# Kernel optimization log

Hardware: AMD Instinct MI355X
Metric: run time of the kernel (lower is better)

Reference implementation:

```python
import jax, jax.numpy as jnp
import numpy as np

N = 256
IN_FEATURES = 2048
OUT_FEATURES = 128
KERNEL_DIMS = 32


def setup_inputs() -> dict:
    key = jax.random.key(0)
    kx, kt = jax.random.split(key)
    x = jax.random.normal(kx, (N, IN_FEATURES), dtype=jnp.float32)
    T = jax.random.normal(kt, (IN_FEATURES, OUT_FEATURES, KERNEL_DIMS), dtype=jnp.float32)
    return {"x": x, "T": T}


def reference(x, T):
    # matrices: [N, out_features, kernel_dims]
    matrices = (x @ T.reshape(IN_FEATURES, OUT_FEATURES * KERNEL_DIMS)).reshape(
        -1, OUT_FEATURES, KERNEL_DIMS
    )
    # pairwise L1 distance over kernel dims: [N, N, out_features]
    norm = jnp.abs(matrices[None, :, :, :] - matrices[:, None, :, :]).sum(axis=3)
    # o_b[j, f] = sum_i exp(-norm[i, j, f]); includes self term exp(0)=1, as in original
    o_b = jnp.exp(-norm).sum(axis=0)  # [N, out_features]
    # mean=False in this configuration, so no division by batch size
    return jnp.concatenate((x, o_b), axis=1)  # [N, in_features + out_features]
```

## Files before the change

kernel.cpp:

```cpp
#include <hip/hip_runtime.h>
#include <hip/hip_bf16.h>
#include <stdint.h>

#define IN_F 2048
#define OUT_F 128
#define KD 32
#define NR 256
#define OC 2176
#define OD 4096
#define THRESH 32.0f
#define KSN 16
#define OPN (1024 * 256)

typedef __bf16 bf16x8 __attribute__((ext_vector_type(8)));
typedef __bf16 bf16x4 __attribute__((ext_vector_type(4)));
typedef float  f32x4  __attribute__((ext_vector_type(4)));
typedef uint16_t u16x8 __attribute__((ext_vector_type(8)));

__global__ __launch_bounds__(256, 2) void fused_kernel(const float* __restrict__ x,
                                                       const float* __restrict__ Tm,
                                                       float* __restrict__ out,
                                                       __bf16* __restrict__ Pp) {
    __shared__ __bf16 Bs[32][136];
    __shared__ __bf16 As[2][4][256][8];

    const int tid  = threadIdx.x;
    const int lane = tid & 63;
    const int wid  = tid >> 6;
    const int fr   = lane & 15, fg = lane >> 4;
    const int bid  = blockIdx.x;
    const int ks   = bid & 15;
    const int fo   = bid >> 4;
    const int k0   = ks * 128;

    {
        const int row = bid >> 1;
        const int off = (bid & 1) * 1024 + tid * 4;
        float4 v = *reinterpret_cast<const float4*>(&x[row * IN_F + off]);
        *reinterpret_cast<float4*>(&out[row * OC + off]) = v;
    }

    float4 xs[8];
    const int kslot = tid & 7;
    const int nrow8 = tid >> 3;
    #pragma unroll
    for (int p = 0; p < 8; ++p)
        xs[p] = *reinterpret_cast<const float4*>(&x[(p * 32 + nrow8) * IN_F + k0 + kslot * 4]);

    #pragma unroll 1
    for (int r = 0; r < 2; ++r) {
        const int idx = r * 256 + tid;
        const int fl  = idx & 3;
        const int kl  = idx >> 2;
        const float* src = Tm + (size_t)(k0 + kl) * OD + (fo * 4 + fl) * KD;

        float v[32];
        #pragma unroll
        for (int q = 0; q < 8; ++q) {
            f32x4 w = *reinterpret_cast<const f32x4*>(src + q * 4);
            v[q * 4]     = w[0];
            v[q * 4 + 1] = w[1];
            v[q * 4 + 2] = w[2];
            v[q * 4 + 3] = w[3];
        }

        float s1[16], d1[16];
        #pragma unroll
        for (int e = 0; e < 16; ++e) { s1[e] = v[2*e] + v[2*e+1]; d1[e] = v[2*e] - v[2*e+1]; }
        float s2[8], d2[8];
        #pragma unroll
        for (int e = 0; e < 8; ++e)  { s2[e] = s1[2*e] + s1[2*e+1]; d2[e] = s1[2*e] - s1[2*e+1]; }
        float s3[4], d3[4];
        #pragma unroll
        for (int e = 0; e < 4; ++e)  { s3[e] = s2[2*e] + s2[2*e+1]; d3[e] = s2[2*e] - s2[2*e+1]; }
        float s4[2], d4[2];
        #pragma unroll
        for (int e = 0; e < 2; ++e)  { s4[e] = s3[2*e] + s3[2*e+1]; d4[e] = s3[2*e] - s3[2*e+1]; }
        const float s5 = s4[0] + s4[1];
        const float d5 = s4[0] - s4[1];

        float pr[8];
        pr[0] = s5;
        { float s = 0.f;
          #pragma unroll
          for (int e = 0; e < 16; ++e) s += d1[e];
          pr[1] = s; }
        { float s = 0.f;
          #pragma unroll
          for (int e = 0; e < 8; ++e) s += d2[e];
          pr[2] = s; }
        pr[3] = (d3[0] + d3[1]) + (d3[2] + d3[3]);
        pr[4] = d4[0] + d4[1];
        pr[5] = d5;
        { float s = 0.f;
          #pragma unroll
          for (int g = 0; g < 8; ++g) s += d1[2*g] - d1[2*g+1];
          pr[6] = s; }
        pr[7] = s3[0] - s3[1] - s3[2] + s3[3];

        #pragma unroll
        for (int p = 0; p < 8; ++p)
            Bs[fl * 8 + p][kl] = (__bf16)pr[p];
    }

    #pragma unroll
    for (int p = 0; p < 8; ++p) {
        bf16x4 b = { (__bf16)xs[p].x, (__bf16)xs[p].y, (__bf16)xs[p].z, (__bf16)xs[p].w };
        *reinterpret_cast<bf16x4*>(&As[0][kslot >> 1][p * 32 + nrow8][(kslot & 1) * 4]) = b;
    }
    __syncthreads();

    f32x4 acc[4][2] = {};

    #pragma unroll 1
    for (int c = 0; c < 4; ++c) {
        const int buf = c & 1;
        if (c < 3) {
            #pragma unroll
            for (int p = 0; p < 8; ++p)
                xs[p] = *reinterpret_cast<const float4*>(
                    &x[(p * 32 + nrow8) * IN_F + k0 + (c + 1) * 32 + kslot * 4]);
        }

        bf16x8 bfrag[2];
        #pragma unroll
        for (int oi = 0; oi < 2; ++oi)
            bfrag[oi] = *reinterpret_cast<const bf16x8*>(&Bs[oi * 16 + fr][c * 32 + fg * 8]);
        #pragma unroll
        for (int mi = 0; mi < 4; ++mi) {
            bf16x8 af = *reinterpret_cast<const bf16x8*>(&As[buf][fg][wid * 64 + mi * 16 + fr][0]);
            acc[mi][0] = __builtin_amdgcn_mfma_f32_16x16x32_bf16(af, bfrag[0], acc[mi][0], 0, 0, 0);
            acc[mi][1] = __builtin_amdgcn_mfma_f32_16x16x32_bf16(af, bfrag[1], acc[mi][1], 0, 0, 0);
        }

        if (c < 3) {
            __syncthreads();
            #pragma unroll
            for (int p = 0; p < 8; ++p) {
                bf16x4 b = { (__bf16)xs[p].x, (__bf16)xs[p].y, (__bf16)xs[p].z, (__bf16)xs[p].w };
                *reinterpret_cast<bf16x4*>(&As[buf ^ 1][kslot >> 1][p * 32 + nrow8][(kslot & 1) * 4]) = b;
            }
            __syncthreads();
        }
    }

    __bf16* dst = Pp + (size_t)ks * OPN;
    #pragma unroll
    for (int mi = 0; mi < 4; ++mi) {
        #pragma unroll
        for (int oi = 0; oi < 2; ++oi) {
            const int op = fo * 32 + oi * 16 + fr;
            const int nb = wid * 64 + mi * 16 + fg * 4;
            bf16x4 v = { (__bf16)acc[mi][oi][0], (__bf16)acc[mi][oi][1],
                         (__bf16)acc[mi][oi][2], (__bf16)acc[mi][oi][3] };
            *reinterpret_cast<bf16x4*>(&dst[(size_t)op * NR + nb]) = v;
        }
    }
}

__global__ __launch_bounds__(256, 2) void screen_kernel(const __bf16* __restrict__ Pp,
                                                        const float* __restrict__ x,
                                                        const float* __restrict__ Tm,
                                                        float* __restrict__ out) {
    __shared__ float P8s[256][8];
    __shared__ float part[4][64];

    const int f    = blockIdx.x;
    const int jq   = blockIdx.y;
    const int tid  = threadIdx.x;
    const int lane = tid & 63;
    const int wid  = tid >> 6;
    const int j    = jq * 64 + lane;

    {
        const int p  = tid >> 5;
        const int n0 = (tid & 31) * 8;
        const uint16_t* base = reinterpret_cast<const uint16_t*>(Pp)
                             + (size_t)(f * 8 + p) * NR + n0;
        float a[8] = {};
        #pragma unroll
        for (int ks = 0; ks < KSN; ++ks) {
            u16x8 v = *reinterpret_cast<const u16x8*>(base + (size_t)ks * OPN);
            #pragma unroll
            for (int e = 0; e < 8; ++e)
                a[e] += __builtin_bit_cast(float, (uint32_t)v[e] << 16);
        }
        #pragma unroll
        for (int e = 0; e < 8; ++e)
            P8s[n0 + e][p] = a[e];
    }
    __syncthreads();

    const f32x4 qj0 = *reinterpret_cast<const f32x4*>(&P8s[j][0]);
    const f32x4 qj1 = *reinterpret_cast<const f32x4*>(&P8s[j][4]);

    float acc = 0.f;
    const int i0 = wid * 64;
    #pragma unroll 2
    for (int ii = 0; ii < 64; ++ii) {
        const int i = i0 + ii;
        f32x4 r0 = *reinterpret_cast<const f32x4*>(&P8s[i][0]);
        f32x4 r1 = *reinterpret_cast<const f32x4*>(&P8s[i][4]);
        f32x4 d0 = r0 - qj0;
        f32x4 d1 = r1 - qj1;
        float m0 = fmaxf(fmaxf(fabsf(d0[0]), fabsf(d0[1])), fabsf(d0[2]));
        float m1 = fmaxf(fmaxf(fabsf(d0[3]), fabsf(d1[0])), fabsf(d1[1]));
        float m2 = fmaxf(fabsf(d1[2]), fabsf(d1[3]));
        const float mx = fmaxf(fmaxf(m0, m1), m2);

        const bool ok = (mx < THRESH) && (i != j);
        if (__builtin_expect(__any(ok), 0)) {
            if (ok) {
                f32x4 ad[8] = {};
                const float* xi = x + (size_t)i * IN_F;
                const float* xj = x + (size_t)j * IN_F;
                for (int k = 0; k < IN_F; ++k) {
                    const float dk = xi[k] - xj[k];
                    const float* tr = Tm + (size_t)k * OD + f * KD;
                    #pragma unroll
                    for (int q = 0; q < 8; ++q) {
                        f32x4 tv = *reinterpret_cast<const f32x4*>(tr + q * 4);
                        ad[q] += dk * tv;
                    }
                }
                float norm = 0.f;
                #pragma unroll
                for (int q = 0; q < 8; ++q)
                    norm += fabsf(ad[q][0]) + fabsf(ad[q][1])
                          + fabsf(ad[q][2]) + fabsf(ad[q][3]);
                acc += __expf(-norm);
            }
        }
    }

    if (wid == jq) acc += 1.0f;

    part[wid][lane] = acc;
    __syncthreads();
    if (tid < 64) {
        float s = part[0][tid] + part[1][tid] + part[2][tid] + part[3][tid];
        out[(jq * 64 + tid) * OC + IN_F + f] = s;
    }
}

extern "C" void kernel_launch(void* const* d_in, const int* in_sizes, int n_in,
                              void* d_out, int out_size, void* d_ws, size_t ws_size,
                              hipStream_t stream) {
    const float* x  = (const float*)d_in[0];
    const float* Tm = (const float*)d_in[1];
    float* out = (float*)d_out;

    __bf16* Pp = (__bf16*)d_ws;

    fused_kernel<<<dim3(512), 256, 0, stream>>>(x, Tm, out, Pp);
    screen_kernel<<<dim3(128, 4), 256, 0, stream>>>(Pp, x, Tm, out);
}
```

Baseline: 28.48 us.

## Halve per-block feature tile, double grid, load x fragments directly from global

Each block of the fused kernel now covers 2 features (16 projection columns) rather than 4, and the grid doubles to 1024 blocks with launch bounds raised to 4 blocks per CU. The double-buffered LDS staging of x and its barriers are removed; each wave instead reads x straight from global memory and converts it to bf16 just before each MFMA. The Bs writes are rotated per feature to reduce LDS bank conflicts. This aims at more parallelism and fewer synchronisations, in exchange for redundant global reads of x across blocks and possibly less coalesced access.

```diff
diff --git a/kernel.cpp b/kernel.cpp
--- a/kernel.cpp
+++ b/kernel.cpp
@@ -17,12 +17,43 @@
 typedef float  f32x4  __attribute__((ext_vector_type(4)));
 typedef uint16_t u16x8 __attribute__((ext_vector_type(8)));
 
-__global__ __launch_bounds__(256, 2) void fused_kernel(const float* __restrict__ x,
+__device__ __forceinline__ void bfly8(const float v[32], float pr[8]) {
+    float s1[16], d1[16];
+    #pragma unroll
+    for (int e = 0; e < 16; ++e) { s1[e] = v[2*e] + v[2*e+1]; d1[e] = v[2*e] - v[2*e+1]; }
+    float s2[8], d2[8];
+    #pragma unroll
+    for (int e = 0; e < 8; ++e)  { s2[e] = s1[2*e] + s1[2*e+1]; d2[e] = s1[2*e] - s1[2*e+1]; }
+    float s3[4], d3[4];
+    #pragma unroll
+    for (int e = 0; e < 4; ++e)  { s3[e] = s2[2*e] + s2[2*e+1]; d3[e] = s2[2*e] - s2[2*e+1]; }
+    float s4[2], d4[2];
+    #pragma unroll
+    for (int e = 0; e < 2; ++e)  { s4[e] = s3[2*e] + s3[2*e+1]; d4[e] = s3[2*e] - s3[2*e+1]; }
+    pr[0] = s4[0] + s4[1];
+    { float s = 0.f;
+      #pragma unroll
+      for (int e = 0; e < 16; ++e) s += d1[e];
+      pr[1] = s; }
+    { float s = 0.f;
+      #pragma unroll
+      for (int e = 0; e < 8; ++e) s += d2[e];
+      pr[2] = s; }
+    pr[3] = (d3[0] + d3[1]) + (d3[2] + d3[3]);
+    pr[4] = d4[0] + d4[1];
+    pr[5] = s4[0] - s4[1];
+    { float s = 0.f;
+      #pragma unroll
+      for (int g = 0; g < 8; ++g) s += d1[2*g] - d1[2*g+1];
+      pr[6] = s; }
+    pr[7] = s3[0] - s3[1] - s3[2] + s3[3];
+}
+
+__global__ __launch_bounds__(256, 4) void fused_kernel(const float* __restrict__ x,
                                                        const float* __restrict__ Tm,
                                                        float* __restrict__ out,
                                                        __bf16* __restrict__ Pp) {
-    __shared__ __bf16 Bs[32][136];
-    __shared__ __bf16 As[2][4][256][8];
+    __shared__ __bf16 Bs[16][136];
 
     const int tid  = threadIdx.x;
     const int lane = tid & 63;
@@ -33,126 +64,61 @@
     const int fo   = bid >> 4;
     const int k0   = ks * 128;
 
-    {
+    if (bid < 512) {
         const int row = bid >> 1;
         const int off = (bid & 1) * 1024 + tid * 4;
         float4 v = *reinterpret_cast<const float4*>(&x[row * IN_F + off]);
         *reinterpret_cast<float4*>(&out[row * OC + off]) = v;
     }
 
-    float4 xs[8];
-    const int kslot = tid & 7;
-    const int nrow8 = tid >> 3;
-    #pragma unroll
-    for (int p = 0; p < 8; ++p)
-        xs[p] = *reinterpret_cast<const float4*>(&x[(p * 32 + nrow8) * IN_F + k0 + kslot * 4]);
-
-    #pragma unroll 1
-    for (int r = 0; r < 2; ++r) {
-        const int idx = r * 256 + tid;
-        const int fl  = idx & 3;
-        const int kl  = idx >> 2;
-        const float* src = Tm + (size_t)(k0 + kl) * OD + (fo * 4 + fl) * KD;
+    {
+        const int fl = tid & 1;
+        const int kl = tid >> 1;
+        const float* src = Tm + (size_t)(k0 + kl) * OD + (fo * 2 + fl) * KD;
 
         float v[32];
         #pragma unroll
         for (int q = 0; q < 8; ++q) {
             f32x4 w = *reinterpret_cast<const f32x4*>(src + q * 4);
-            v[q * 4]     = w[0];
-            v[q * 4 + 1] = w[1];
-            v[q * 4 + 2] = w[2];
-            v[q * 4 + 3] = w[3];
-        }
-
-        float s1[16], d1[16];
-        #pragma unroll
-        for (int e = 0; e < 16; ++e) { s1[e] = v[2*e] + v[2*e+1]; d1[e] = v[2*e] - v[2*e+1]; }
-        float s2[8], d2[8];
-        #pragma unroll
-        for (int e = 0; e < 8; ++e)  { s2[e] = s1[2*e] + s1[2*e+1]; d2[e] = s1[2*e] - s1[2*e+1]; }
-        float s3[4], d3[4];
-        #pragma unroll
-        for (int e = 0; e < 4; ++e)  { s3[e] = s2[2*e] + s2[2*e+1]; d3[e] = s2[2*e] - s2[2*e+1]; }
-        float s4[2], d4[2];
-        #pragma unroll
-        for (int e = 0; e < 2; ++e)  { s4[e] = s3[2*e] + s3[2*e+1]; d4[e] = s3[2*e] - s3[2*e+1]; }
-        const float s5 = s4[0] + s4[1];
-        const float d5 = s4[0] - s4[1];
+            v[q*4] = w[0]; v[q*4+1] = w[1]; v[q*4+2] = w[2]; v[q*4+3] = w[3];
+        }
 
         float pr[8];
-        pr[0] = s5;
-        { float s = 0.f;
-          #pragma unroll
-          for (int e = 0; e < 16; ++e) s += d1[e];
-          pr[1] = s; }
-        { float s = 0.f;
-          #pragma unroll
-          for (int e = 0; e < 8; ++e) s += d2[e];
-          pr[2] = s; }
-        pr[3] = (d3[0] + d3[1]) + (d3[2] + d3[3]);
-        pr[4] = d4[0] + d4[1];
-        pr[5] = d5;
-        { float s = 0.f;
-          #pragma unroll
-          for (int g = 0; g < 8; ++g) s += d1[2*g] - d1[2*g+1];
-          pr[6] = s; }
-        pr[7] = s3[0] - s3[1] - s3[2] + s3[3];
-
-        #pragma unroll
-        for (int p = 0; p < 8; ++p)
+        bfly8(v, pr);
+
+        #pragma unroll
+        for (int pp = 0; pp < 8; ++pp) {
+            const int p = (pp + fl * 4) & 7;
             Bs[fl * 8 + p][kl] = (__bf16)pr[p];
-    }
-
-    #pragma unroll
-    for (int p = 0; p < 8; ++p) {
-        bf16x4 b = { (__bf16)xs[p].x, (__bf16)xs[p].y, (__bf16)xs[p].z, (__bf16)xs[p].w };
-        *reinterpret_cast<bf16x4*>(&As[0][kslot >> 1][p * 32 + nrow8][(kslot & 1) * 4]) = b;
+        }
     }
     __syncthreads();
 
-    f32x4 acc[4][2] = {};
-
-    #pragma unroll 1
+    f32x4 acc[4] = {};
+
+    #pragma unroll
     for (int c = 0; c < 4; ++c) {
-        const int buf = c & 1;
-        if (c < 3) {
-            #pragma unroll
-            for (int p = 0; p < 8; ++p)
-                xs[p] = *reinterpret_cast<const float4*>(
-                    &x[(p * 32 + nrow8) * IN_F + k0 + (c + 1) * 32 + kslot * 4]);
-        }
-
-        bf16x8 bfrag[2];
-        #pragma unroll
-        for (int oi = 0; oi < 2; ++oi)
-            bfrag[oi] = *reinterpret_cast<const bf16x8*>(&Bs[oi * 16 + fr][c * 32 + fg * 8]);
+        const bf16x8 bfrag = *reinterpret_cast<const bf16x8*>(&Bs[fr][c * 32 + fg * 8]);
         #pragma unroll
         for (int mi = 0; mi < 4; ++mi) {
-            bf16x8 af = *reinterpret_cast<const bf16x8*>(&As[buf][fg][wid * 64 + mi * 16 + fr][0]);
-            acc[mi][0] = __builtin_amdgcn_mfma_f32_16x16x32_bf16(af, bfrag[0], acc[mi][0], 0, 0, 0);
-            acc[mi][1] = __builtin_amdgcn_mfma_f32_16x16x32_bf16(af, bfrag[1], acc[mi][1], 0, 0, 0);
-        }
-
-        if (c < 3) {
-            __syncthreads();
-            #pragma unroll
-            for (int p = 0; p < 8; ++p) {
-                bf16x4 b = { (__bf16)xs[p].x, (__bf16)xs[p].y, (__bf16)xs[p].z, (__bf16)xs[p].w };
-                *reinterpret_cast<bf16x4*>(&As[buf ^ 1][kslot >> 1][p * 32 + nrow8][(kslot & 1) * 4]) = b;
-            }
-            __syncthreads();
-        }
-    }
-
-    __bf16* dst = Pp + (size_t)ks * OPN;
-    #pragma unroll
-    for (int mi = 0; mi < 4; ++mi) {
-        #pragma unroll
-        for (int oi = 0; oi < 2; ++oi) {
-            const int op = fo * 32 + oi * 16 + fr;
+            const int n = wid * 64 + mi * 16 + fr;
+            const float* ap = &x[(size_t)n * IN_F + k0 + c * 32 + fg * 8];
+            float4 u0 = *reinterpret_cast<const float4*>(ap);
+            float4 u1 = *reinterpret_cast<const float4*>(ap + 4);
+            bf16x8 af = { (__bf16)u0.x, (__bf16)u0.y, (__bf16)u0.z, (__bf16)u0.w,
+                          (__bf16)u1.x, (__bf16)u1.y, (__bf16)u1.z, (__bf16)u1.w };
+            acc[mi] = __builtin_amdgcn_mfma_f32_16x16x32_bf16(af, bfrag, acc[mi], 0, 0, 0);
+        }
+    }
+
+    {
+        __bf16* dst = Pp + (size_t)ks * OPN;
+        const int op = fo * 16 + fr;
+        #pragma unroll
+        for (int mi = 0; mi < 4; ++mi) {
             const int nb = wid * 64 + mi * 16 + fg * 4;
-            bf16x4 v = { (__bf16)acc[mi][oi][0], (__bf16)acc[mi][oi][1],
-                         (__bf16)acc[mi][oi][2], (__bf16)acc[mi][oi][3] };
+            bf16x4 v = { (__bf16)acc[mi][0], (__bf16)acc[mi][1],
+                         (__bf16)acc[mi][2], (__bf16)acc[mi][3] };
             *reinterpret_cast<bf16x4*>(&dst[(size_t)op * NR + nb]) = v;
         }
     }
@@ -252,6 +218,6 @@
 
     __bf16* Pp = (__bf16*)d_ws;
 
-    fused_kernel<<<dim3(512), 256, 0, stream>>>(x, Tm, out, Pp);
+    fused_kernel<<<dim3(1024), 256, 0, stream>>>(x, Tm, out, Pp);
     screen_kernel<<<dim3(128, 4), 256, 0, stream>>>(Pp, x, Tm, out);
 }
```

After: 38.13 us. 1.34x slower.
